# Kernel tuning notes

Hardware: AMD Instinct MI355X
Metric: run time of the kernel (lower is better)

Reference implementation:

```python
import jax, jax.numpy as jnp
import numpy as np

B, C, H, W = 4, 64, 160, 160
K = 3
KK = K * K
PAD = (K - 1) // 2
EPS = 1e-5


def conv2d(x, w, b):
    y = jax.lax.conv_general_dilated(
        x, w, (1, 1), [(PAD, PAD), (PAD, PAD)],
        dimension_numbers=('NCHW', 'OIHW', 'NCHW'))
    return y + b[None, :, None, None]


def batchnorm(x, g, b, m, v):
    # eval-mode BN with running stats
    return (x - m[None, :, None, None]) * jax.lax.rsqrt(v + EPS)[None, :, None, None] * g[None, :, None, None] + b[None, :, None, None]


def bilinear_gather(x, py, px):
    # x: [B,C,H,W]; py,px: [B,KK,H,W] float sample coords -> [B,C,KK,H,W]
    Bx, Cx, Hx, Wx = x.shape
    y0 = jnp.floor(py)
    x0 = jnp.floor(px)
    ly = py - y0
    lx = px - x0
    x_flat = x.reshape(Bx, Cx, 1, Hx * Wx)
    acc = jnp.zeros((Bx, Cx, py.shape[1], Hx * Wx), dtype=x.dtype)
    corners = ((y0, x0, (1 - ly) * (1 - lx)),
               (y0, x0 + 1, (1 - ly) * lx),
               (y0 + 1, x0, ly * (1 - lx)),
               (y0 + 1, x0 + 1, ly * lx))
    for yi, xi, wgt in corners:
        valid = (yi >= 0) & (yi < Hx) & (xi >= 0) & (xi < Wx)
        yc = jnp.clip(yi, 0, Hx - 1).astype(jnp.int32)
        xc = jnp.clip(xi, 0, Wx - 1).astype(jnp.int32)
        idx = (yc * Wx + xc).reshape(Bx, -1, Hx * Wx)          # [B,KK,HW]
        g = jnp.take_along_axis(x_flat, idx[:, None], axis=3)  # [B,C,KK,HW]
        acc = acc + (wgt * valid).reshape(Bx, 1, -1, Hx * Wx) * g
    return acc.reshape(Bx, Cx, -1, Hx, Wx)


def modulated_deform_conv(x, offset, mask, weight):
    # x:[B,C,H,W] offset:[B,2*KK,H,W] (mmcv layout: pairs (dy,dx) interleaved) mask:[B,KK,H,W]
    Bx, Cx, Hx, Wx = x.shape
    Co = weight.shape[0]
    off = offset.reshape(Bx, KK, 2, Hx, Wx)
    k = jnp.arange(KK)
    ki = (k // K).astype(x.dtype)
    kj = (k % K).astype(x.dtype)
    ys = jnp.arange(Hx, dtype=x.dtype)
    xs = jnp.arange(Wx, dtype=x.dtype)
    py = ys[None, None, :, None] - PAD + ki[None, :, None, None] + off[:, :, 0]
    px = xs[None, None, None, :] - PAD + kj[None, :, None, None] + off[:, :, 1]
    samp = bilinear_gather(x, py, px)            # [B,C,KK,H,W]
    samp = samp * mask[:, None]                  # modulation
    return jnp.einsum('bckhw,ock->bohw', samp, weight.reshape(Co, Cx, KK))


def setup_inputs() -> dict:
    key = jax.random.key(0)
    ks = jax.random.split(key, 16)
    inp = {
        'x': jax.random.normal(ks[0], (B, C, H, W), jnp.float32),
        'w_om1': jax.random.normal(ks[1], (3 * KK, C, K, K), jnp.float32) * 0.01,
        'b_om1': jax.random.normal(ks[2], (3 * KK,), jnp.float32) * 0.01,
        'w_dcn1': jax.random.normal(ks[3], (C, C, K, K), jnp.float32) * 0.04,
        'bn1_g': jax.random.uniform(ks[4], (C,), jnp.float32, 0.5, 1.5),
        'bn1_b': jax.random.normal(ks[5], (C,), jnp.float32) * 0.1,
        'bn1_m': jax.random.normal(ks[6], (C,), jnp.float32) * 0.1,
        'bn1_v': jax.random.uniform(ks[7], (C,), jnp.float32, 0.5, 1.5),
        'w_om2': jax.random.normal(ks[8], (3 * KK, C, K, K), jnp.float32) * 0.01,
        'b_om2': jax.random.normal(ks[9], (3 * KK,), jnp.float32) * 0.01,
        'w_dcn2': jax.random.normal(ks[10], (C, C, K, K), jnp.float32) * 0.04,
        'bn2_g': jax.random.uniform(ks[11], (C,), jnp.float32, 0.5, 1.5),
        'bn2_b': jax.random.normal(ks[12], (C,), jnp.float32) * 0.1,
        'bn2_m': jax.random.normal(ks[13], (C,), jnp.float32) * 0.1,
        'bn2_v': jax.random.uniform(ks[14], (C,), jnp.float32, 0.5, 1.5),
    }
    return inp


def reference(x, w_om1, b_om1, w_dcn1, bn1_g, bn1_b, bn1_m, bn1_v,
              w_om2, b_om2, w_dcn2, bn2_g, bn2_b, bn2_m, bn2_v):
    identity = x
    om1 = conv2d(x, w_om1, b_om1)
    o1, o2, m1 = jnp.split(om1, 3, axis=1)
    offset1 = jnp.concatenate([o1, o2], axis=1)
    mask1 = jax.nn.sigmoid(m1)
    out = modulated_deform_conv(x, offset1, mask1, w_dcn1)
    out = batchnorm(out, bn1_g, bn1_b, bn1_m, bn1_v)
    out = jax.nn.gelu(out, approximate=False)
    om2 = conv2d(out, w_om2, b_om2)
    o1b, o2b, m2 = jnp.split(om2, 3, axis=1)
    offset2 = jnp.concatenate([o1b, o2b], axis=1)
    mask2 = jax.nn.sigmoid(m2)
    out = modulated_deform_conv(out, offset2, mask2, w_dcn2)
    out = batchnorm(out, bn2_g, bn2_b, bn2_m, bn2_v)
    out = out + identity
    return jax.nn.gelu(out, approximate=False)
```

## Files before the change

### kernel.cpp

```cpp
#include <hip/hip_runtime.h>
#include <math.h>

#define HH 160
#define WW 160
#define HWSZ 25600
#define TR 10
#define TC 22
#define NSLOT 220

typedef __attribute__((ext_vector_type(8))) short short8;
typedef __attribute__((ext_vector_type(4))) short short4v;
typedef __attribute__((ext_vector_type(8))) _Float16 half8;
typedef __attribute__((ext_vector_type(2))) _Float16 half2v;
typedef __attribute__((ext_vector_type(4))) float f32x4;

__device__ __forceinline__ short f2h(float f) {
  union { _Float16 h; short s; } u; u.h = (_Float16)f; return u.s;
}
__device__ __forceinline__ float h2f(short s) {
  union { _Float16 h; short s; } u; u.s = s; return (float)u.h;
}
__device__ __forceinline__ half2v bcast_h(short s) {
  unsigned int x = (unsigned short)s; x |= x << 16;
  union { unsigned int u; half2v h; } v; v.u = x; return v.h;
}

__global__ __launch_bounds__(256) void pre_kernel(
    const float* __restrict__ x,
    const float* __restrict__ g1, const float* __restrict__ b1,
    const float* __restrict__ m1, const float* __restrict__ v1,
    const float* __restrict__ g2, const float* __restrict__ b2,
    const float* __restrict__ m2, const float* __restrict__ v2,
    const float* __restrict__ wd1, const float* __restrict__ wd2,
    const float* __restrict__ wo1, const float* __restrict__ wo2,
    float* __restrict__ sc, short* __restrict__ wd1h, short* __restrict__ wd2h,
    short* __restrict__ wo1h, short* __restrict__ wo2h,
    short* __restrict__ xcl) {
  __shared__ short tmp[64][72];
  int t = threadIdx.x;
  int bx = blockIdx.x;
  if (bx < 1600) {
    int b = bx / 400, p0 = (bx - b * 400) * 64;
    const float* xb = x + (size_t)b * 64 * HWSZ;
    for (int i = t; i < 4096; i += 256) {
      int c = i >> 6, p = i & 63;
      tmp[p][c] = f2h(xb[c * HWSZ + p0 + p]);
    }
    __syncthreads();
    short* ob = xcl + ((size_t)b * HWSZ + p0) * 64;
    for (int i = t; i < 512; i += 256) {
      int p = i >> 3, g = i & 7;
      *(short8*)&ob[p * 64 + g * 8] = *(const short8*)&tmp[p][g * 8];
    }
    return;
  }
  int i0 = (bx - 1600) * 256 + t;
  for (int i = i0; i < 36864; i += 16384) {
    int j = i & 7, q = (i >> 3) & 3, m = (i >> 5) & 15;
    int ot = (i >> 9) & 3, f = i >> 11;
    int kp = f * 32 + q * 8 + j;
    int k = kp >> 6, c = kp & 63;
    int src = (ot * 16 + m) * 576 + c * 9 + k;
    wd1h[i] = f2h(wd1[src]);
    wd2h[i] = f2h(wd2[src]);
  }
  for (int i = i0; i < 18432; i += 16384) {
    int j = i & 7, q = (i >> 3) & 3, m = (i >> 5) & 15;
    int ot = (i >> 9) & 1, f = i >> 10;
    int kp = f * 32 + q * 8 + j;
    int k = kp >> 6, c = kp & 63;
    int oc = ot * 16 + m;
    wo1h[i] = (oc < 27) ? f2h(wo1[oc * 576 + c * 9 + k]) : (short)0;
    wo2h[i] = (oc < 27) ? f2h(wo2[oc * 576 + c * 9 + k]) : (short)0;
  }
  if (i0 < 64) {
    float s1 = g1[i0] * rsqrtf(v1[i0] + 1e-5f);
    sc[i0]       = s1;
    sc[64 + i0]  = b1[i0] - m1[i0] * s1;
    float s2 = g2[i0] * rsqrtf(v2[i0] + 1e-5f);
    sc[128 + i0] = s2;
    sc[192 + i0] = b2[i0] - m2[i0] * s2;
  }
}

__global__ __launch_bounds__(256, 5) void dcn_fused(
    const short* __restrict__ xcl,
    const short* __restrict__ who,
    const float* __restrict__ bias_om,
    const short* __restrict__ whd,
    const float* __restrict__ scale, const float* __restrict__ shift,
    const short* __restrict__ id_cl,
    short* __restrict__ out_cl,
    float* __restrict__ out_f32) {
  __shared__ short xt[NSLOT * 64];
  __shared__ __align__(16) short As[2304];

  int t = threadIdx.x;
  int x0 = blockIdx.x * 16, y0 = blockIdx.y * 4, b = blockIdx.z;
  int w = t >> 6, lane = t & 63, q = lane >> 4, m = lane & 15;
  int ybase = y0 - 3, xbase = x0 - 3;

  const short* xb = xcl + (size_t)b * HWSZ * 64;
  for (int i = t; i < NSLOT * 8; i += 256) {
    int slot = i >> 3, g = i & 7;
    int ty = slot / TC, tx = slot - ty * TC;
    int gy = ybase + ty, gx = xbase + tx;
    short8 v = {};
    if (gy >= 0 && gy < HH && gx >= 0 && gx < WW)
      v = *(const short8*)&xb[(gy * WW + gx) * 64 + g * 8];
    *(short8*)&xt[slot * 64 + ((g ^ (slot & 7)) << 3)] = v;
  }
  __syncthreads();

  {
    f32x4 oacc0 = {}, oacc1 = {};
#pragma unroll 6
    for (int f = 0; f < 18; f++) {
      int k = f >> 1;
      int ki = k / 3, kj = k - ki * 3;
      int g = (f & 1) * 4 + q;
      int slotb = (w + ki + 2) * TC + (m + kj + 2);
      short8 bv = *(const short8*)&xt[slotb * 64 + ((g ^ (slotb & 7)) << 3)];
      const short* ap = who + (f * 128 + m * 4 + q) * 8;
      short8 a0 = *(const short8*)ap;
      short8 a1 = *(const short8*)(ap + 512);
      union { short8 s8; half8 h; } A0, A1, B;
      A0.s8 = a0; A1.s8 = a1; B.s8 = bv;
      oacc0 = __builtin_amdgcn_mfma_f32_16x16x32_f16(A0.h, B.h, oacc0, 0, 0, 0);
      oacc1 = __builtin_amdgcn_mfma_f32_16x16x32_f16(A1.h, B.h, oacc1, 0, 0, 0);
    }
    int px = w * 16 + m;
#pragma unroll
    for (int mt = 0; mt < 2; mt++) {
      f32x4 oa = mt ? oacc1 : oacc0;
      short4v pv;
#pragma unroll
      for (int r = 0; r < 4; r++) {
        int oc = mt * 16 + q * 4 + r;
        float bb = (oc < 27) ? bias_om[oc] : 0.f;
        pv[r] = f2h(oa[r] + bb);
      }
      *(short4v*)&As[px * 36 + mt * 16 + q * 4] = pv;
    }
  }
  __syncthreads();

  union { short s[36]; short4v v4[9]; } omr;
  {
    int px = w * 16 + m;
#pragma unroll
    for (int i = 0; i < 9; i++)
      omr.v4[i] = *(const short4v*)&As[px * 36 + i * 4];
  }

  f32x4 acc[4] = {};
#pragma unroll
  for (int k = 0; k < 9; k++) {
    int y = y0 + w, x = x0 + m;
    float dy = h2f(omr.s[2 * k]);
    float dx = h2f(omr.s[2 * k + 1]);
    float ml = h2f(omr.s[18 + k]);
    float msk = 1.f / (1.f + __expf(-ml));
    int ki = k / 3, kj = k - ki * 3;
    float py  = (float)(y - 1 + ki) + dy;
    float pxf = (float)(x - 1 + kj) + dx;
    float fy = floorf(py), fx = floorf(pxf);
    float ly = py - fy, lx = pxf - fx;
    int yi0 = (int)fy, xi0 = (int)fx;
    bool vy0 = (yi0 >= 0) & (yi0 < HH), vy1 = (yi0 + 1 >= 0) & (yi0 + 1 < HH);
    bool vx0 = (xi0 >= 0) & (xi0 < WW), vx1 = (xi0 + 1 >= 0) & (xi0 + 1 < WW);
    int ty0 = min(max(yi0 - ybase, 0), TR - 2);
    int tx0 = min(max(xi0 - xbase, 0), TC - 2);
    int p00 = ty0 * TC + tx0;
    half2v w00 = bcast_h(f2h((vy0 & vx0) ? (1.f - ly) * (1.f - lx) * msk : 0.f));
    half2v w01 = bcast_h(f2h((vy0 & vx1) ? (1.f - ly) * lx * msk : 0.f));
    half2v w10 = bcast_h(f2h((vy1 & vx0) ? ly * (1.f - lx) * msk : 0.f));
    half2v w11 = bcast_h(f2h((vy1 & vx1) ? ly * lx * msk : 0.f));
    int s00 = p00, s01 = p00 + 1, s10 = p00 + TC, s11 = p00 + TC + 1;
    const short* wk = whd + k * 4096 + m * 32 + q * 8;
#pragma unroll
    for (int ch = 0; ch < 2; ch++) {
      int g = ch * 4 + q;
      const short* ap = wk + ch * 2048;
      short8 a0 = *(const short8*)ap;
      short8 a1 = *(const short8*)(ap + 512);
      short8 a2 = *(const short8*)(ap + 1024);
      short8 a3 = *(const short8*)(ap + 1536);
      union { short8 s8; half2v h[4]; } c00, c01, c10, c11, bb;
      c00.s8 = *(const short8*)&xt[s00 * 64 + ((g ^ (s00 & 7)) << 3)];
      c01.s8 = *(const short8*)&xt[s01 * 64 + ((g ^ (s01 & 7)) << 3)];
      c10.s8 = *(const short8*)&xt[s10 * 64 + ((g ^ (s10 & 7)) << 3)];
      c11.s8 = *(const short8*)&xt[s11 * 64 + ((g ^ (s11 & 7)) << 3)];
#pragma unroll
      for (int d = 0; d < 4; d++)
        bb.h[d] = c00.h[d] * w00 + c01.h[d] * w01 + c10.h[d] * w10 +
                  c11.h[d] * w11;
      union { short8 s8; half8 h8; } B, A0, A1, A2, A3;
      B.s8 = bb.s8; A0.s8 = a0; A1.s8 = a1; A2.s8 = a2; A3.s8 = a3;
      acc[0] = __builtin_amdgcn_mfma_f32_16x16x32_f16(A0.h8, B.h8, acc[0], 0, 0, 0);
      acc[1] = __builtin_amdgcn_mfma_f32_16x16x32_f16(A1.h8, B.h8, acc[1], 0, 0, 0);
      acc[2] = __builtin_amdgcn_mfma_f32_16x16x32_f16(A2.h8, B.h8, acc[2], 0, 0, 0);
      acc[3] = __builtin_amdgcn_mfma_f32_16x16x32_f16(A3.h8, B.h8, acc[3], 0, 0, 0);
    }
  }

  int y = y0 + w, x = x0 + m;
  if (out_f32) {
    size_t pbase = ((size_t)b * HWSZ + y * WW + x) * 64;
#pragma unroll
    for (int ot = 0; ot < 4; ot++) {
      short4v iv = *(const short4v*)&id_cl[pbase + ot * 16 + q * 4];
#pragma unroll
      for (int r = 0; r < 4; r++) {
        int oc = ot * 16 + q * 4 + r;
        size_t idx = ((size_t)(b * 64 + oc)) * HWSZ + y * WW + x;
        float v = acc[ot][r] * scale[oc] + shift[oc] + h2f(iv[r]);
        v = 0.5f * v * (1.f + erff(v * 0.70710678118654752f));
        out_f32[idx] = v;
      }
    }
  } else {
    size_t base = ((size_t)b * HWSZ + y * WW + x) * 64;
#pragma unroll
    for (int ot = 0; ot < 4; ot++) {
      short4v pv;
#pragma unroll
      for (int r = 0; r < 4; r++) {
        int oc = ot * 16 + q * 4 + r;
        float v = acc[ot][r] * scale[oc] + shift[oc];
        v = 0.5f * v * (1.f + erff(v * 0.70710678118654752f));
        pv[r] = f2h(v);
      }
      *(short4v*)&out_cl[base + ot * 16 + q * 4] = pv;
    }
  }
}

extern "C" void kernel_launch(void* const* d_in, const int* in_sizes, int n_in,
                              void* d_out, int out_size, void* d_ws, size_t ws_size,
                              hipStream_t stream) {
  const float* x     = (const float*)d_in[0];
  const float* w_om1 = (const float*)d_in[1];
  const float* b_om1 = (const float*)d_in[2];
  const float* w_d1  = (const float*)d_in[3];
  const float* bn1g  = (const float*)d_in[4];
  const float* bn1b  = (const float*)d_in[5];
  const float* bn1m  = (const float*)d_in[6];
  const float* bn1v  = (const float*)d_in[7];
  const float* w_om2 = (const float*)d_in[8];
  const float* b_om2 = (const float*)d_in[9];
  const float* w_d2  = (const float*)d_in[10];
  const float* bn2g  = (const float*)d_in[11];
  const float* bn2b  = (const float*)d_in[12];
  const float* bn2m  = (const float*)d_in[13];
  const float* bn2v  = (const float*)d_in[14];

  float* ws    = (float*)d_ws;
  float* sc    = ws;
  short* w1h   = (short*)(ws + 256);
  short* w2h   = w1h + 36864;
  short* wo1h  = w2h + 36864;
  short* wo2h  = wo1h + 18432;
  short* x_cl  = (short*)(ws + 55552);
  short* o1_cl = x_cl + 6553600;
  float* outp  = (float*)d_out;

  pre_kernel<<<dim3(1664), dim3(256), 0, stream>>>(
      x, bn1g, bn1b, bn1m, bn1v, bn2g, bn2b, bn2m, bn2v,
      w_d1, w_d2, w_om1, w_om2, sc, w1h, w2h, wo1h, wo2h, x_cl);

  dim3 grid(WW / 16, HH / 4, 4);
  dcn_fused<<<grid, dim3(256), 0, stream>>>(
      x_cl, wo1h, b_om1, w1h, sc, sc + 64, nullptr, o1_cl, nullptr);
  dcn_fused<<<grid, dim3(256), 0, stream>>>(
      o1_cl, wo2h, b_om2, w2h, sc + 128, sc + 192, x_cl, nullptr, outp);
}
```

Baseline: 220.1 us.

## Stage deform-conv weights through double-buffered LDS with register prefetch

The per-tap DCN weight slices (4096 halves per kernel tap) are now prefetched into registers one tap ahead and written into a double-buffered LDS area, so the MFMA A-operands come from LDS instead of global memory. The weight prep kernel reorders its layout (m before q) so each thread's cooperative 8-element copy lines up with the LDS read pattern. Identity loads for the residual are hoisted before the main loop, and launch bounds are relaxed from 5 to 3 waves per SIMD. This adds a block barrier per tap, more LDS per block and lower occupancy in exchange for avoiding repeated global/L2 weight fetches.

```diff
diff --git a/kernel.cpp b/kernel.cpp
--- a/kernel.cpp
+++ b/kernel.cpp
@@ -56,7 +56,7 @@
   }
   int i0 = (bx - 1600) * 256 + t;
   for (int i = i0; i < 36864; i += 16384) {
-    int j = i & 7, q = (i >> 3) & 3, m = (i >> 5) & 15;
+    int j = i & 7, m = (i >> 3) & 15, q = (i >> 7) & 3;
     int ot = (i >> 9) & 3, f = i >> 11;
     int kp = f * 32 + q * 8 + j;
     int k = kp >> 6, c = kp & 63;
@@ -83,7 +83,7 @@
   }
 }
 
-__global__ __launch_bounds__(256, 5) void dcn_fused(
+__global__ __launch_bounds__(256, 3) void dcn_fused(
     const short* __restrict__ xcl,
     const short* __restrict__ who,
     const float* __restrict__ bias_om,
@@ -93,12 +93,16 @@
     short* __restrict__ out_cl,
     float* __restrict__ out_f32) {
   __shared__ short xt[NSLOT * 64];
-  __shared__ __align__(16) short As[2304];
+  __shared__ __align__(16) short Asd[8192];
+  __shared__ __align__(16) short oms[2304];
 
   int t = threadIdx.x;
   int x0 = blockIdx.x * 16, y0 = blockIdx.y * 4, b = blockIdx.z;
   int w = t >> 6, lane = t & 63, q = lane >> 4, m = lane & 15;
   int ybase = y0 - 3, xbase = x0 - 3;
+
+  short8 pr0 = *(const short8*)&whd[t * 8];
+  short8 pr1 = *(const short8*)&whd[2048 + t * 8];
 
   const short* xb = xcl + (size_t)b * HWSZ * 64;
   for (int i = t; i < NSLOT * 8; i += 256) {
@@ -110,6 +114,10 @@
       v = *(const short8*)&xb[(gy * WW + gx) * 64 + g * 8];
     *(short8*)&xt[slot * 64 + ((g ^ (slot & 7)) << 3)] = v;
   }
+  *(short8*)&Asd[t * 8]        = pr0;
+  *(short8*)&Asd[2048 + t * 8] = pr1;
+  pr0 = *(const short8*)&whd[4096 + t * 8];
+  pr1 = *(const short8*)&whd[4096 + 2048 + t * 8];
   __syncthreads();
 
   {
@@ -140,7 +148,7 @@
         float bb = (oc < 27) ? bias_om[oc] : 0.f;
         pv[r] = f2h(oa[r] + bb);
       }
-      *(short4v*)&As[px * 36 + mt * 16 + q * 4] = pv;
+      *(short4v*)&oms[px * 36 + mt * 16 + q * 4] = pv;
     }
   }
   __syncthreads();
@@ -150,13 +158,33 @@
     int px = w * 16 + m;
 #pragma unroll
     for (int i = 0; i < 9; i++)
-      omr.v4[i] = *(const short4v*)&As[px * 36 + i * 4];
+      omr.v4[i] = *(const short4v*)&oms[px * 36 + i * 4];
+  }
+
+  int y = y0 + w, x = x0 + m;
+
+  short4v ivs[4];
+  if (out_f32) {
+    size_t pbase = ((size_t)b * HWSZ + y * WW + x) * 64;
+#pragma unroll
+    for (int ot = 0; ot < 4; ot++)
+      ivs[ot] = *(const short4v*)&id_cl[pbase + ot * 16 + q * 4];
   }
 
   f32x4 acc[4] = {};
 #pragma unroll
   for (int k = 0; k < 9; k++) {
-    int y = y0 + w, x = x0 + m;
+    const short* rbuf = Asd + (k & 1) * 4096;
+    if (k < 8) {
+      short* wbuf = Asd + ((k & 1) ^ 1) * 4096;
+      *(short8*)&wbuf[t * 8]        = pr0;
+      *(short8*)&wbuf[2048 + t * 8] = pr1;
+    }
+    if (k < 7) {
+      pr0 = *(const short8*)&whd[(k + 2) * 4096 + t * 8];
+      pr1 = *(const short8*)&whd[(k + 2) * 4096 + 2048 + t * 8];
+    }
+
     float dy = h2f(omr.s[2 * k]);
     float dx = h2f(omr.s[2 * k + 1]);
     float ml = h2f(omr.s[18 + k]);
@@ -177,11 +205,10 @@
     half2v w10 = bcast_h(f2h((vy1 & vx0) ? ly * (1.f - lx) * msk : 0.f));
     half2v w11 = bcast_h(f2h((vy1 & vx1) ? ly * lx * msk : 0.f));
     int s00 = p00, s01 = p00 + 1, s10 = p00 + TC, s11 = p00 + TC + 1;
-    const short* wk = whd + k * 4096 + m * 32 + q * 8;
 #pragma unroll
     for (int ch = 0; ch < 2; ch++) {
       int g = ch * 4 + q;
-      const short* ap = wk + ch * 2048;
+      const short* ap = rbuf + ch * 2048 + (q * 16 + m) * 8;
       short8 a0 = *(const short8*)ap;
       short8 a1 = *(const short8*)(ap + 512);
       short8 a2 = *(const short8*)(ap + 1024);
@@ -202,19 +229,17 @@
       acc[2] = __builtin_amdgcn_mfma_f32_16x16x32_f16(A2.h8, B.h8, acc[2], 0, 0, 0);
       acc[3] = __builtin_amdgcn_mfma_f32_16x16x32_f16(A3.h8, B.h8, acc[3], 0, 0, 0);
     }
-  }
-
-  int y = y0 + w, x = x0 + m;
+    if (k < 8) __syncthreads();
+  }
+
   if (out_f32) {
-    size_t pbase = ((size_t)b * HWSZ + y * WW + x) * 64;
 #pragma unroll
     for (int ot = 0; ot < 4; ot++) {
-      short4v iv = *(const short4v*)&id_cl[pbase + ot * 16 + q * 4];
 #pragma unroll
       for (int r = 0; r < 4; r++) {
         int oc = ot * 16 + q * 4 + r;
         size_t idx = ((size_t)(b * 64 + oc)) * HWSZ + y * WW + x;
-        float v = acc[ot][r] * scale[oc] + shift[oc] + h2f(iv[r]);
+        float v = acc[ot][r] * scale[oc] + shift[oc] + h2f(ivs[ot][r]);
         v = 0.5f * v * (1.f + erff(v * 0.70710678118654752f));
         out_f32[idx] = v;
       }
```

After: 200.9 us. 1.1x faster.
